# Kernel optimization log

Measured on AMD Instinct MI355X. Metric: run time of the kernel, lower is better.

Reference implementation:

```python
import jax, jax.numpy as jnp
import numpy as np

N_NODES = 50000
N_EDGES = 800000
DIM_IN, DIM_H, DIM_OUT = 128, 128, 64


def _init_linear(key, fan_in, fan_out):
    # kaiming-uniform-ish init, matches torch Linear scale
    lim = 1.0 / np.sqrt(fan_in)
    return jax.random.uniform(key, (fan_in, fan_out), jnp.float32, -lim, lim)


def setup_inputs() -> dict:
    key = jax.random.key(0)
    ks = jax.random.split(key, 12)
    x = jax.random.normal(ks[0], (N_NODES, DIM_IN), jnp.float32)
    edge_index = jax.random.randint(ks[1], (2, N_EDGES), 0, N_NODES, jnp.int32)
    dims = [(DIM_IN, DIM_H), (DIM_H, DIM_H), (DIM_H, DIM_OUT)]
    inp = {"x": x, "edge_index": edge_index}
    for i, (fi, fo) in enumerate(dims):
        inp[f"Wl{i}"] = _init_linear(ks[2 + 3 * i], fi, fo)   # neighbor transform
        inp[f"Wr{i}"] = _init_linear(ks[3 + 3 * i], fi, fo)   # root transform
        inp[f"b{i}"] = jnp.zeros((fo,), jnp.float32)
    return inp


def _sage_layer(x, src, dst, Wl, Wr, b):
    # mean aggregation of neighbor messages x[src] at destination nodes
    msg = x[src]                                              # [E, d]
    agg = jax.ops.segment_sum(msg, dst, num_segments=N_NODES)  # [N, d]
    cnt = jax.ops.segment_sum(jnp.ones((src.shape[0],), x.dtype), dst,
                              num_segments=N_NODES)
    mean = agg / jnp.maximum(cnt, 1.0)[:, None]               # isolated nodes -> 0
    return mean @ Wl + b + x @ Wr                              # SAGEConv


def reference(x, edge_index, Wl0, Wr0, b0, Wl1, Wr1, b1, Wl2, Wr2, b2):
    src, dst = edge_index[0], edge_index[1]
    layers = [(Wl0, Wr0, b0), (Wl1, Wr1, b1), (Wl2, Wr2, b2)]
    h = x
    for i, (Wl, Wr, b) in enumerate(layers):
        h = _sage_layer(h, src, dst, Wl, Wr, b)
        if i != len(layers) - 1:
            h = jax.nn.relu(h)  # dropout p=0.2 is identity in eval mode
    return jax.nn.log_softmax(h, axis=1), h
```

## Files before the change

kernel.cpp:

```cpp
#include <hip/hip_runtime.h>

#define N_NODES 50000
#define N_EDGES 800000
#define SCAN_BLOCKS 196
#define WIN 6250

typedef __attribute__((ext_vector_type(8))) short short8;
typedef __attribute__((ext_vector_type(4))) float f32x4;
typedef unsigned short ushort_t;
typedef unsigned int uint_t;

__device__ inline ushort_t f2bf(float f) {
    union { float f; uint_t u; } v; v.f = f;
    uint_t u = v.u;
    u += 0x7fffu + ((u >> 16) & 1u);
    return (ushort_t)(u >> 16);
}
__device__ inline float bflo(uint_t v) { return __uint_as_float(v << 16); }
__device__ inline float bfhi(uint_t v) { return __uint_as_float(v & 0xffff0000u); }
__device__ inline float bf2f(ushort_t v) { return __uint_as_float((uint_t)v << 16); }

__global__ void prep(const float* __restrict__ x, uint_t* __restrict__ x_bf_u,
                     const float* __restrict__ Wl0, const float* __restrict__ Wr0,
                     const float* __restrict__ Wl1, const float* __restrict__ Wr1,
                     const float* __restrict__ Wl2, const float* __restrict__ Wr2,
                     ushort_t* __restrict__ pk0, ushort_t* __restrict__ pk1,
                     ushort_t* __restrict__ pkz, int* __restrict__ cnt) {
    int b = blockIdx.x, tid = threadIdx.x;
    if (b < 6250) {
        int i = b * 256 + tid;
        float4 v = ((const float4*)x)[i];
        uint_t lo = (uint_t)f2bf(v.x) | ((uint_t)f2bf(v.y) << 16);
        uint_t hi = (uint_t)f2bf(v.z) | ((uint_t)f2bf(v.w) << 16);
        x_bf_u[i * 2] = lo; x_bf_u[i * 2 + 1] = hi;
    } else if (b < 6506) {
        int bb = b - 6250;
        const float* Wl = (bb < 128) ? Wl0 : Wl1;
        const float* Wr = (bb < 128) ? Wr0 : Wr1;
        ushort_t* out = (bb < 128) ? pk0 : pk1;
        int idx = (bb & 127) * 256 + tid;
        int j = idx & 7, l = (idx >> 3) & 63, t = (idx >> 9) & 7, ks = idx >> 12;
        int n = t * 16 + (l & 15);
        int k = ks * 32 + (l >> 4) * 8 + j;
        float w = (k < 128) ? Wl[k * 128 + n] : Wr[(k - 128) * 128 + n];
        out[idx] = f2bf(w);
    } else if (b < 6570) {
        int idx = (b - 6506) * 256 + tid;
        int j = idx & 7, l = (idx >> 3) & 63, t = (idx >> 9) & 7, ks = idx >> 12;
        int n = t * 16 + (l & 15);
        int k = ks * 32 + (l >> 4) * 8 + j;
        float w = (n < 64) ? Wl2[k * 64 + n] : Wr2[k * 64 + (n - 64)];
        pkz[idx] = f2bf(w);
    } else {
        int i = (b - 6570) * 256 + tid;
        if (i < 12500) ((int4*)cnt)[i] = make_int4(0, 0, 0, 0);
    }
}

__global__ void count_edges_mp(const int* __restrict__ ei, int* __restrict__ cnt) {
    int g = blockIdx.x & 7;
    int nb = gridDim.x >> 3;
    int bi = blockIdx.x >> 3;
    int lo = g * WIN;
    for (int e = bi * 256 + threadIdx.x; e < N_EDGES; e += nb * 256) {
        int d = ei[N_EDGES + e];
        if ((unsigned)(d - lo) < WIN) atomicAdd(&cnt[d], 1);
    }
}

__global__ void fill_csr_mp(const int* __restrict__ ei, int* __restrict__ cursor,
                            int* __restrict__ csr_src) {
    int g = blockIdx.x & 7;
    int nb = gridDim.x >> 3;
    int bi = blockIdx.x >> 3;
    int lo = g * WIN;
    for (int e = bi * 256 + threadIdx.x; e < N_EDGES; e += nb * 256) {
        int d = ei[N_EDGES + e];
        if ((unsigned)(d - lo) < WIN) {
            int p = atomicAdd(&cursor[d], 1);
            csr_src[p] = ei[e];
        }
    }
}

__global__ void scan_all(const int* __restrict__ cnt, int* __restrict__ rowstart,
                         int* __restrict__ cursor) {
    __shared__ int s[256];
    __shared__ int wsum[4];
    int t = threadIdx.x, b = blockIdx.x;
    int base = b * 256;
    int pre = 0;
    for (int i = t; i < base; i += 256) pre += cnt[i];
    for (int off = 32; off; off >>= 1) pre += __shfl_down(pre, off, 64);
    if ((t & 63) == 0) wsum[t >> 6] = pre;
    __syncthreads();
    int prefix_base = wsum[0] + wsum[1] + wsum[2] + wsum[3];
    int i = base + t;
    int v = (i < N_NODES) ? cnt[i] : 0;
    s[t] = v;
    __syncthreads();
    for (int off = 1; off < 256; off <<= 1) {
        int add = (t >= off) ? s[t - off] : 0;
        __syncthreads();
        s[t] += add;
        __syncthreads();
    }
    int excl = s[t] - v + prefix_base;
    if (i < N_NODES) { rowstart[i] = excl; cursor[i] = excl; }
    if (b == 0 && t == 0) rowstart[N_NODES] = N_EDGES;
}

__device__ inline void gather_mean(const uint_t* __restrict__ base,
                                   const int* __restrict__ rowstart,
                                   const int* __restrict__ csr_src,
                                   int node, int lane, float& ax, float& ay) {
    int s0 = rowstart[node], s1 = rowstart[node + 1];
    ax = 0.f; ay = 0.f;
    for (int b = s0; b < s1; b += 64) {
        int m = min(64, s1 - b);
        int idx = (lane < m) ? csr_src[b + lane] : 0;
        int j = 0;
        for (; j + 8 <= m; j += 8) {
            uint_t v0 = base[(size_t)__shfl(idx, j + 0, 64) * 64 + lane];
            uint_t v1 = base[(size_t)__shfl(idx, j + 1, 64) * 64 + lane];
            uint_t v2 = base[(size_t)__shfl(idx, j + 2, 64) * 64 + lane];
            uint_t v3 = base[(size_t)__shfl(idx, j + 3, 64) * 64 + lane];
            uint_t v4 = base[(size_t)__shfl(idx, j + 4, 64) * 64 + lane];
            uint_t v5 = base[(size_t)__shfl(idx, j + 5, 64) * 64 + lane];
            uint_t v6 = base[(size_t)__shfl(idx, j + 6, 64) * 64 + lane];
            uint_t v7 = base[(size_t)__shfl(idx, j + 7, 64) * 64 + lane];
            ax += ((bflo(v0) + bflo(v1)) + (bflo(v2) + bflo(v3)))
                + ((bflo(v4) + bflo(v5)) + (bflo(v6) + bflo(v7)));
            ay += ((bfhi(v0) + bfhi(v1)) + (bfhi(v2) + bfhi(v3)))
                + ((bfhi(v4) + bfhi(v5)) + (bfhi(v6) + bfhi(v7)));
        }
        for (; j < m; ++j) {
            uint_t v = base[(size_t)__shfl(idx, j, 64) * 64 + lane];
            ax += bflo(v);
            ay += bfhi(v);
        }
    }
    float inv = 1.0f / fmaxf((float)(s1 - s0), 1.0f);
    ax *= inv; ay *= inv;
}

template <bool CHAIN>
__global__ __launch_bounds__(256) void layer_fused(
    const uint_t* __restrict__ gsrc, const ushort_t* __restrict__ root,
    const int* __restrict__ rowstart, const int* __restrict__ csr_src,
    const ushort_t* __restrict__ Bpk, const float* __restrict__ bias1,
    const ushort_t* __restrict__ Bpkz, const float* __restrict__ bias2,
    ushort_t* __restrict__ h_out,
    ushort_t* __restrict__ z_bf, float* __restrict__ r_f32) {
    __shared__ ushort_t At[16 * 136];
    int lane = threadIdx.x & 63, wave = threadIdx.x >> 6;
    int nodeBase = blockIdx.x * 16;

    #pragma unroll
    for (int i = 0; i < 4; ++i) {
        int m = wave * 4 + i;
        int node = nodeBase + m;
        float ax = 0.f, ay = 0.f;
        if (node < N_NODES) gather_mean(gsrc, rowstart, csr_src, node, lane, ax, ay);
        ((uint_t*)(At + m * 136))[lane] = (uint_t)f2bf(ax) | ((uint_t)f2bf(ay) << 16);
    }
    __syncthreads();

    int row16 = lane & 15, quad = lane >> 4;
    const short8* bp = (const short8*)Bpk + lane;
    int rootRow = min(nodeBase + row16, N_NODES - 1);
    const ushort_t* rrow = root + (size_t)rootRow * 128;

    f32x4 acc[2];
    #pragma unroll
    for (int tt = 0; tt < 2; ++tt) { f32x4 z = {0.f, 0.f, 0.f, 0.f}; acc[tt] = z; }

    #pragma unroll
    for (int ks = 0; ks < 8; ++ks) {
        short8 afrag;
        if (ks < 4) afrag = *(const short8*)&At[row16 * 136 + ks * 32 + quad * 8];
        else        afrag = *(const short8*)(rrow + (ks - 4) * 32 + quad * 8);
        #pragma unroll
        for (int tt = 0; tt < 2; ++tt) {
            int t = wave * 2 + tt;
            short8 bfrag = bp[(ks * 8 + t) * 64];
            acc[tt] = __builtin_amdgcn_mfma_f32_16x16x32_bf16(afrag, bfrag, acc[tt], 0, 0, 0);
        }
    }

    if (!CHAIN) {
        #pragma unroll
        for (int tt = 0; tt < 2; ++tt) {
            int col = (wave * 2 + tt) * 16 + row16;
            float bv = bias1[col];
            #pragma unroll
            for (int r = 0; r < 4; ++r) {
                int row = nodeBase + quad * 4 + r;
                if (row < N_NODES) {
                    float v = fmaxf(acc[tt][r] + bv, 0.f);
                    h_out[(size_t)row * 128 + col] = f2bf(v);
                }
            }
        }
    } else {
        __syncthreads();
        #pragma unroll
        for (int tt = 0; tt < 2; ++tt) {
            int col = (wave * 2 + tt) * 16 + row16;
            float bv = bias1[col];
            #pragma unroll
            for (int r = 0; r < 4; ++r) {
                float v = fmaxf(acc[tt][r] + bv, 0.f);
                At[(quad * 4 + r) * 136 + col] = f2bf(v);
            }
        }
        __syncthreads();

        const short8* bpz = (const short8*)Bpkz + lane;
        f32x4 accz[2];
        #pragma unroll
        for (int tt = 0; tt < 2; ++tt) { f32x4 z = {0.f, 0.f, 0.f, 0.f}; accz[tt] = z; }

        #pragma unroll
        for (int ks = 0; ks < 4; ++ks) {
            short8 afrag = *(const short8*)&At[row16 * 136 + ks * 32 + quad * 8];
            #pragma unroll
            for (int tt = 0; tt < 2; ++tt) {
                int t = wave * 2 + tt;
                short8 bfrag = bpz[(ks * 8 + t) * 64];
                accz[tt] = __builtin_amdgcn_mfma_f32_16x16x32_bf16(afrag, bfrag, accz[tt], 0, 0, 0);
            }
        }

        #pragma unroll
        for (int tt = 0; tt < 2; ++tt) {
            int col = (wave * 2 + tt) * 16 + row16;
            #pragma unroll
            for (int r = 0; r < 4; ++r) {
                int row = nodeBase + quad * 4 + r;
                if (row < N_NODES) {
                    if (col < 64) z_bf[(size_t)row * 64 + col] = f2bf(accz[tt][r]);
                    else          r_f32[(size_t)row * 64 + (col - 64)] = accz[tt][r] + bias2[col - 64];
                }
            }
        }
    }
}

__global__ void final_agg_softmax(const ushort_t* __restrict__ z_bf,
                                  const float* __restrict__ r_f32,
                                  const int* __restrict__ rowstart,
                                  const int* __restrict__ csr_src,
                                  float* __restrict__ out) {
    int node = blockIdx.x * 4 + (threadIdx.x >> 6);
    int lane = threadIdx.x & 63;
    if (node >= N_NODES) return;
    int s0 = rowstart[node], s1 = rowstart[node + 1];
    float a = 0.f;
    for (int b = s0; b < s1; b += 64) {
        int m = min(64, s1 - b);
        int idx = (lane < m) ? csr_src[b + lane] : 0;
        int j = 0;
        for (; j + 8 <= m; j += 8) {
            float v0 = bf2f(z_bf[(size_t)__shfl(idx, j + 0, 64) * 64 + lane]);
            float v1 = bf2f(z_bf[(size_t)__shfl(idx, j + 1, 64) * 64 + lane]);
            float v2 = bf2f(z_bf[(size_t)__shfl(idx, j + 2, 64) * 64 + lane]);
            float v3 = bf2f(z_bf[(size_t)__shfl(idx, j + 3, 64) * 64 + lane]);
            float v4 = bf2f(z_bf[(size_t)__shfl(idx, j + 4, 64) * 64 + lane]);
            float v5 = bf2f(z_bf[(size_t)__shfl(idx, j + 5, 64) * 64 + lane]);
            float v6 = bf2f(z_bf[(size_t)__shfl(idx, j + 6, 64) * 64 + lane]);
            float v7 = bf2f(z_bf[(size_t)__shfl(idx, j + 7, 64) * 64 + lane]);
            a += ((v0 + v1) + (v2 + v3)) + ((v4 + v5) + (v6 + v7));
        }
        for (; j < m; ++j)
            a += bf2f(z_bf[(size_t)__shfl(idx, j, 64) * 64 + lane]);
    }
    float inv = 1.0f / fmaxf((float)(s1 - s0), 1.0f);
    float h = a * inv + r_f32[(size_t)node * 64 + lane];
    float mx = h;
    for (int off = 32; off; off >>= 1) mx = fmaxf(mx, __shfl_xor(mx, off, 64));
    float e = expf(h - mx);
    float s = e;
    for (int off = 32; off; off >>= 1) s += __shfl_xor(s, off, 64);
    float lse = mx + logf(s);
    out[(size_t)node * 64 + lane] = h - lse;
    out[(size_t)N_NODES * 64 + (size_t)node * 64 + lane] = h;
}

extern "C" void kernel_launch(void* const* d_in, const int* in_sizes, int n_in,
                              void* d_out, int out_size, void* d_ws, size_t ws_size,
                              hipStream_t stream) {
    const float* x  = (const float*)d_in[0];
    const int* ei   = (const int*)d_in[1];
    const float* Wl0 = (const float*)d_in[2];
    const float* Wr0 = (const float*)d_in[3];
    const float* b0  = (const float*)d_in[4];
    const float* Wl1 = (const float*)d_in[5];
    const float* Wr1 = (const float*)d_in[6];
    const float* b1  = (const float*)d_in[7];
    const float* Wl2 = (const float*)d_in[8];
    const float* Wr2 = (const float*)d_in[9];
    const float* b2  = (const float*)d_in[10];
    float* out = (float*)d_out;

    char* ws = (char*)d_ws;
    int* cnt      = (int*)(ws + 0x000000);
    int* rowstart = (int*)(ws + 0x040000);
    int* cursor   = (int*)(ws + 0x080000);
    int* csr_src  = (int*)(ws + 0x100000);
    ushort_t* pk0 = (ushort_t*)(ws + 0x420000);
    ushort_t* pk1 = (ushort_t*)(ws + 0x440000);
    ushort_t* pkz = (ushort_t*)(ws + 0x460000);
    ushort_t* x_bf = (ushort_t*)(ws + 0x0500000);
    ushort_t* h1   = (ushort_t*)(ws + 0x1F00000);
    ushort_t* z_bf = (ushort_t*)(ws + 0x1200000);
    float*    r_f32 = (float*)  (ws + 0x0500000);

    prep<<<6619, 256, 0, stream>>>(x, (uint_t*)x_bf, Wl0, Wr0, Wl1, Wr1, Wl2, Wr2,
                                   pk0, pk1, pkz, cnt);

    count_edges_mp<<<1024, 256, 0, stream>>>(ei, cnt);
    scan_all<<<SCAN_BLOCKS, 256, 0, stream>>>(cnt, rowstart, cursor);
    fill_csr_mp<<<1024, 256, 0, stream>>>(ei, cursor, csr_src);

    layer_fused<false><<<3125, 256, 0, stream>>>(
        (const uint_t*)x_bf, x_bf, rowstart, csr_src, pk0, b0,
        nullptr, nullptr, h1, nullptr, nullptr);

    layer_fused<true><<<3125, 256, 0, stream>>>(
        (const uint_t*)h1, h1, rowstart, csr_src, pk1, b1,
        pkz, b2, nullptr, z_bf, r_f32);

    final_agg_softmax<<<12500, 256, 0, stream>>>(z_bf, r_f32, rowstart, csr_src, out);
}
```

Measured before the change: 330.9 us.

## Gather neighbor rows with 16-byte vector loads and split waves across edges

Neighbor aggregation now loads each feature row as uint4 chunks, so one wave covers four edges at once (eight in the final kernel) and the partial sums are combined with cross-lane shuffles. The fused layer kernels move to 512 threads with 8 waves, each wave gathering 2 nodes and computing a single 16-column MFMA tile. The goal is fewer, wider memory transactions and more memory-level parallelism in the gather-bound phases. The cost is extra shuffle reductions, partly idle lanes on tails and for low-degree nodes, and higher register pressure under the new launch bounds.

New measurement: 337.4 us. Within noise of the previous version (+1.9%).

```diff
diff --git a/kernel.cpp b/kernel.cpp
--- a/kernel.cpp
+++ b/kernel.cpp
@@ -18,7 +18,9 @@
 }
 __device__ inline float bflo(uint_t v) { return __uint_as_float(v << 16); }
 __device__ inline float bfhi(uint_t v) { return __uint_as_float(v & 0xffff0000u); }
-__device__ inline float bf2f(ushort_t v) { return __uint_as_float((uint_t)v << 16); }
+__device__ inline uint_t packbf(float a, float b) {
+    return (uint_t)f2bf(a) | ((uint_t)f2bf(b) << 16);
+}
 
 __global__ void prep(const float* __restrict__ x, uint_t* __restrict__ x_bf_u,
                      const float* __restrict__ Wl0, const float* __restrict__ Wr0,
@@ -30,9 +32,8 @@
     if (b < 6250) {
         int i = b * 256 + tid;
         float4 v = ((const float4*)x)[i];
-        uint_t lo = (uint_t)f2bf(v.x) | ((uint_t)f2bf(v.y) << 16);
-        uint_t hi = (uint_t)f2bf(v.z) | ((uint_t)f2bf(v.w) << 16);
-        x_bf_u[i * 2] = lo; x_bf_u[i * 2 + 1] = hi;
+        x_bf_u[i * 2] = packbf(v.x, v.y);
+        x_bf_u[i * 2 + 1] = packbf(v.z, v.w);
     } else if (b < 6506) {
         int bb = b - 6250;
         const float* Wl = (bb < 128) ? Wl0 : Wl1;
@@ -110,59 +111,84 @@
     if (b == 0 && t == 0) rowstart[N_NODES] = N_EDGES;
 }
 
-__device__ inline void gather_mean(const uint_t* __restrict__ base,
-                                   const int* __restrict__ rowstart,
-                                   const int* __restrict__ csr_src,
-                                   int node, int lane, float& ax, float& ay) {
+__device__ inline void gather_mean4_128(const uint4* __restrict__ base,
+                                        const int* __restrict__ rowstart,
+                                        const int* __restrict__ csr,
+                                        int node, int lane, float* acc) {
     int s0 = rowstart[node], s1 = rowstart[node + 1];
-    ax = 0.f; ay = 0.f;
+    #pragma unroll
+    for (int k = 0; k < 8; ++k) acc[k] = 0.f;
+    int chunk = lane & 15, esel = lane >> 4;
     for (int b = s0; b < s1; b += 64) {
         int m = min(64, s1 - b);
-        int idx = (lane < m) ? csr_src[b + lane] : 0;
+        int idx = (lane < m) ? csr[b + lane] : 0;
         int j = 0;
-        for (; j + 8 <= m; j += 8) {
-            uint_t v0 = base[(size_t)__shfl(idx, j + 0, 64) * 64 + lane];
-            uint_t v1 = base[(size_t)__shfl(idx, j + 1, 64) * 64 + lane];
-            uint_t v2 = base[(size_t)__shfl(idx, j + 2, 64) * 64 + lane];
-            uint_t v3 = base[(size_t)__shfl(idx, j + 3, 64) * 64 + lane];
-            uint_t v4 = base[(size_t)__shfl(idx, j + 4, 64) * 64 + lane];
-            uint_t v5 = base[(size_t)__shfl(idx, j + 5, 64) * 64 + lane];
-            uint_t v6 = base[(size_t)__shfl(idx, j + 6, 64) * 64 + lane];
-            uint_t v7 = base[(size_t)__shfl(idx, j + 7, 64) * 64 + lane];
-            ax += ((bflo(v0) + bflo(v1)) + (bflo(v2) + bflo(v3)))
-                + ((bflo(v4) + bflo(v5)) + (bflo(v6) + bflo(v7)));
-            ay += ((bfhi(v0) + bfhi(v1)) + (bfhi(v2) + bfhi(v3)))
-                + ((bfhi(v4) + bfhi(v5)) + (bfhi(v6) + bfhi(v7)));
-        }
-        for (; j < m; ++j) {
-            uint_t v = base[(size_t)__shfl(idx, j, 64) * 64 + lane];
-            ax += bflo(v);
-            ay += bfhi(v);
+        for (; j + 16 <= m; j += 16) {
+            int i0 = __shfl(idx, j + esel, 64);
+            int i1 = __shfl(idx, j + 4 + esel, 64);
+            int i2 = __shfl(idx, j + 8 + esel, 64);
+            int i3 = __shfl(idx, j + 12 + esel, 64);
+            uint4 v0 = base[(size_t)i0 * 16 + chunk];
+            uint4 v1 = base[(size_t)i1 * 16 + chunk];
+            uint4 v2 = base[(size_t)i2 * 16 + chunk];
+            uint4 v3 = base[(size_t)i3 * 16 + chunk];
+            acc[0] += (bflo(v0.x) + bflo(v1.x)) + (bflo(v2.x) + bflo(v3.x));
+            acc[1] += (bfhi(v0.x) + bfhi(v1.x)) + (bfhi(v2.x) + bfhi(v3.x));
+            acc[2] += (bflo(v0.y) + bflo(v1.y)) + (bflo(v2.y) + bflo(v3.y));
+            acc[3] += (bfhi(v0.y) + bfhi(v1.y)) + (bfhi(v2.y) + bfhi(v3.y));
+            acc[4] += (bflo(v0.z) + bflo(v1.z)) + (bflo(v2.z) + bflo(v3.z));
+            acc[5] += (bfhi(v0.z) + bfhi(v1.z)) + (bfhi(v2.z) + bfhi(v3.z));
+            acc[6] += (bflo(v0.w) + bflo(v1.w)) + (bflo(v2.w) + bflo(v3.w));
+            acc[7] += (bfhi(v0.w) + bfhi(v1.w)) + (bfhi(v2.w) + bfhi(v3.w));
+        }
+        for (; j < m; j += 4) {
+            int e = j + esel;
+            int s = __shfl(idx, min(e, m - 1), 64);
+            if (e < m) {
+                uint4 v = base[(size_t)s * 16 + chunk];
+                acc[0] += bflo(v.x); acc[1] += bfhi(v.x);
+                acc[2] += bflo(v.y); acc[3] += bfhi(v.y);
+                acc[4] += bflo(v.z); acc[5] += bfhi(v.z);
+                acc[6] += bflo(v.w); acc[7] += bfhi(v.w);
+            }
         }
     }
     float inv = 1.0f / fmaxf((float)(s1 - s0), 1.0f);
-    ax *= inv; ay *= inv;
+    #pragma unroll
+    for (int k = 0; k < 8; ++k) {
+        acc[k] += __shfl_xor(acc[k], 16, 64);
+        acc[k] += __shfl_xor(acc[k], 32, 64);
+        acc[k] *= inv;
+    }
 }
 
 template <bool CHAIN>
-__global__ __launch_bounds__(256) void layer_fused(
-    const uint_t* __restrict__ gsrc, const ushort_t* __restrict__ root,
+__global__ __launch_bounds__(512, 8) void layer_fused(
+    const uint4* __restrict__ gsrc, const ushort_t* __restrict__ root,
     const int* __restrict__ rowstart, const int* __restrict__ csr_src,
     const ushort_t* __restrict__ Bpk, const float* __restrict__ bias1,
     const ushort_t* __restrict__ Bpkz, const float* __restrict__ bias2,
     ushort_t* __restrict__ h_out,
     ushort_t* __restrict__ z_bf, float* __restrict__ r_f32) {
-    __shared__ ushort_t At[16 * 136];
+    __shared__ __align__(16) ushort_t At[16 * 136];
     int lane = threadIdx.x & 63, wave = threadIdx.x >> 6;
     int nodeBase = blockIdx.x * 16;
-
-    #pragma unroll
-    for (int i = 0; i < 4; ++i) {
-        int m = wave * 4 + i;
+    int chunk = lane & 15;
+
+    #pragma unroll
+    for (int i = 0; i < 2; ++i) {
+        int m = wave * 2 + i;
         int node = nodeBase + m;
-        float ax = 0.f, ay = 0.f;
-        if (node < N_NODES) gather_mean(gsrc, rowstart, csr_src, node, lane, ax, ay);
-        ((uint_t*)(At + m * 136))[lane] = (uint_t)f2bf(ax) | ((uint_t)f2bf(ay) << 16);
+        float acc[8];
+        #pragma unroll
+        for (int k = 0; k < 8; ++k) acc[k] = 0.f;
+        if (node < N_NODES) gather_mean4_128(gsrc, rowstart, csr_src, node, lane, acc);
+        if (lane < 16) {
+            uint4 w;
+            w.x = packbf(acc[0], acc[1]); w.y = packbf(acc[2], acc[3]);
+            w.z = packbf(acc[4], acc[5]); w.w = packbf(acc[6], acc[7]);
+            *(uint4*)&At[m * 136 + chunk * 8] = w;
+        }
     }
     __syncthreads();
 
@@ -171,83 +197,58 @@
     int rootRow = min(nodeBase + row16, N_NODES - 1);
     const ushort_t* rrow = root + (size_t)rootRow * 128;
 
-    f32x4 acc[2];
-    #pragma unroll
-    for (int tt = 0; tt < 2; ++tt) { f32x4 z = {0.f, 0.f, 0.f, 0.f}; acc[tt] = z; }
-
+    f32x4 acc1 = {0.f, 0.f, 0.f, 0.f};
     #pragma unroll
     for (int ks = 0; ks < 8; ++ks) {
         short8 afrag;
         if (ks < 4) afrag = *(const short8*)&At[row16 * 136 + ks * 32 + quad * 8];
         else        afrag = *(const short8*)(rrow + (ks - 4) * 32 + quad * 8);
-        #pragma unroll
-        for (int tt = 0; tt < 2; ++tt) {
-            int t = wave * 2 + tt;
-            short8 bfrag = bp[(ks * 8 + t) * 64];
-            acc[tt] = __builtin_amdgcn_mfma_f32_16x16x32_bf16(afrag, bfrag, acc[tt], 0, 0, 0);
-        }
-    }
-
+        short8 bfrag = bp[(ks * 8 + wave) * 64];
+        acc1 = __builtin_amdgcn_mfma_f32_16x16x32_bf16(afrag, bfrag, acc1, 0, 0, 0);
+    }
+
+    int col = wave * 16 + row16;
     if (!CHAIN) {
-        #pragma unroll
-        for (int tt = 0; tt < 2; ++tt) {
-            int col = (wave * 2 + tt) * 16 + row16;
-            float bv = bias1[col];
-            #pragma unroll
-            for (int r = 0; r < 4; ++r) {
-                int row = nodeBase + quad * 4 + r;
-                if (row < N_NODES) {
-                    float v = fmaxf(acc[tt][r] + bv, 0.f);
-                    h_out[(size_t)row * 128 + col] = f2bf(v);
-                }
+        float bv = bias1[col];
+        #pragma unroll
+        for (int r = 0; r < 4; ++r) {
+            int row = nodeBase + quad * 4 + r;
+            if (row < N_NODES) {
+                float v = fmaxf(acc1[r] + bv, 0.f);
+                h_out[(size_t)row * 128 + col] = f2bf(v);
             }
         }
     } else {
         __syncthreads();
-        #pragma unroll
-        for (int tt = 0; tt < 2; ++tt) {
-            int col = (wave * 2 + tt) * 16 + row16;
-            float bv = bias1[col];
-            #pragma unroll
-            for (int r = 0; r < 4; ++r) {
-                float v = fmaxf(acc[tt][r] + bv, 0.f);
-                At[(quad * 4 + r) * 136 + col] = f2bf(v);
-            }
+        float bv = bias1[col];
+        #pragma unroll
+        for (int r = 0; r < 4; ++r) {
+            float v = fmaxf(acc1[r] + bv, 0.f);
+            At[(quad * 4 + r) * 136 + col] = f2bf(v);
         }
         __syncthreads();
 
         const short8* bpz = (const short8*)Bpkz + lane;
-        f32x4 accz[2];
-        #pragma unroll
-        for (int tt = 0; tt < 2; ++tt) { f32x4 z = {0.f, 0.f, 0.f, 0.f}; accz[tt] = z; }
-
+        f32x4 acc2 = {0.f, 0.f, 0.f, 0.f};
         #pragma unroll
         for (int ks = 0; ks < 4; ++ks) {
             short8 afrag = *(const short8*)&At[row16 * 136 + ks * 32 + quad * 8];
-            #pragma unroll
-            for (int tt = 0; tt < 2; ++tt) {
-                int t = wave * 2 + tt;
-                short8 bfrag = bpz[(ks * 8 + t) * 64];
-                accz[tt] = __builtin_amdgcn_mfma_f32_16x16x32_bf16(afrag, bfrag, accz[tt], 0, 0, 0);
+            short8 bfrag = bpz[(ks * 8 + wave) * 64];
+            acc2 = __builtin_amdgcn_mfma_f32_16x16x32_bf16(afrag, bfrag, acc2, 0, 0, 0);
+        }
+
+        #pragma unroll
+        for (int r = 0; r < 4; ++r) {
+            int row = nodeBase + quad * 4 + r;
+            if (row < N_NODES) {
+                if (col < 64) z_bf[(size_t)row * 64 + col] = f2bf(acc2[r]);
+                else          r_f32[(size_t)row * 64 + (col - 64)] = acc2[r] + bias2[col - 64];
             }
         }
-
-        #pragma unroll
-        for (int tt = 0; tt < 2; ++tt) {
-            int col = (wave * 2 + tt) * 16 + row16;
-            #pragma unroll
-            for (int r = 0; r < 4; ++r) {
-                int row = nodeBase + quad * 4 + r;
-                if (row < N_NODES) {
-                    if (col < 64) z_bf[(size_t)row * 64 + col] = f2bf(accz[tt][r]);
-                    else          r_f32[(size_t)row * 64 + (col - 64)] = accz[tt][r] + bias2[col - 64];
-                }
-            }
-        }
-    }
-}
-
-__global__ void final_agg_softmax(const ushort_t* __restrict__ z_bf,
+    }
+}
+
+__global__ void final_agg_softmax(const uint4* __restrict__ zb,
                                   const float* __restrict__ r_f32,
                                   const int* __restrict__ rowstart,
                                   const int* __restrict__ csr_src,
@@ -256,35 +257,81 @@
     int lane = threadIdx.x & 63;
     if (node >= N_NODES) return;
     int s0 = rowstart[node], s1 = rowstart[node + 1];
-    float a = 0.f;
+    int chunk = lane & 7, esel = lane >> 3;
+    float acc[8];
+    #pragma unroll
+    for (int k = 0; k < 8; ++k) acc[k] = 0.f;
     for (int b = s0; b < s1; b += 64) {
         int m = min(64, s1 - b);
         int idx = (lane < m) ? csr_src[b + lane] : 0;
         int j = 0;
-        for (; j + 8 <= m; j += 8) {
-            float v0 = bf2f(z_bf[(size_t)__shfl(idx, j + 0, 64) * 64 + lane]);
-            float v1 = bf2f(z_bf[(size_t)__shfl(idx, j + 1, 64) * 64 + lane]);
-            float v2 = bf2f(z_bf[(size_t)__shfl(idx, j + 2, 64) * 64 + lane]);
-            float v3 = bf2f(z_bf[(size_t)__shfl(idx, j + 3, 64) * 64 + lane]);
-            float v4 = bf2f(z_bf[(size_t)__shfl(idx, j + 4, 64) * 64 + lane]);
-            float v5 = bf2f(z_bf[(size_t)__shfl(idx, j + 5, 64) * 64 + lane]);
-            float v6 = bf2f(z_bf[(size_t)__shfl(idx, j + 6, 64) * 64 + lane]);
-            float v7 = bf2f(z_bf[(size_t)__shfl(idx, j + 7, 64) * 64 + lane]);
-            a += ((v0 + v1) + (v2 + v3)) + ((v4 + v5) + (v6 + v7));
-        }
-        for (; j < m; ++j)
-            a += bf2f(z_bf[(size_t)__shfl(idx, j, 64) * 64 + lane]);
+        for (; j + 32 <= m; j += 32) {
+            int i0 = __shfl(idx, j + esel, 64);
+            int i1 = __shfl(idx, j + 8 + esel, 64);
+            int i2 = __shfl(idx, j + 16 + esel, 64);
+            int i3 = __shfl(idx, j + 24 + esel, 64);
+            uint4 v0 = zb[(size_t)i0 * 8 + chunk];
+            uint4 v1 = zb[(size_t)i1 * 8 + chunk];
+            uint4 v2 = zb[(size_t)i2 * 8 + chunk];
+            uint4 v3 = zb[(size_t)i3 * 8 + chunk];
+            acc[0] += (bflo(v0.x) + bflo(v1.x)) + (bflo(v2.x) + bflo(v3.x));
+            acc[1] += (bfhi(v0.x) + bfhi(v1.x)) + (bfhi(v2.x) + bfhi(v3.x));
+            acc[2] += (bflo(v0.y) + bflo(v1.y)) + (bflo(v2.y) + bflo(v3.y));
+            acc[3] += (bfhi(v0.y) + bfhi(v1.y)) + (bfhi(v2.y) + bfhi(v3.y));
+            acc[4] += (bflo(v0.z) + bflo(v1.z)) + (bflo(v2.z) + bflo(v3.z));
+            acc[5] += (bfhi(v0.z) + bfhi(v1.z)) + (bfhi(v2.z) + bfhi(v3.z));
+            acc[6] += (bflo(v0.w) + bflo(v1.w)) + (bflo(v2.w) + bflo(v3.w));
+            acc[7] += (bfhi(v0.w) + bfhi(v1.w)) + (bfhi(v2.w) + bfhi(v3.w));
+        }
+        for (; j < m; j += 8) {
+            int e = j + esel;
+            int s = __shfl(idx, min(e, m - 1), 64);
+            if (e < m) {
+                uint4 v = zb[(size_t)s * 8 + chunk];
+                acc[0] += bflo(v.x); acc[1] += bfhi(v.x);
+                acc[2] += bflo(v.y); acc[3] += bfhi(v.y);
+                acc[4] += bflo(v.z); acc[5] += bfhi(v.z);
+                acc[6] += bflo(v.w); acc[7] += bfhi(v.w);
+            }
+        }
     }
     float inv = 1.0f / fmaxf((float)(s1 - s0), 1.0f);
-    float h = a * inv + r_f32[(size_t)node * 64 + lane];
-    float mx = h;
-    for (int off = 32; off; off >>= 1) mx = fmaxf(mx, __shfl_xor(mx, off, 64));
-    float e = expf(h - mx);
-    float s = e;
-    for (int off = 32; off; off >>= 1) s += __shfl_xor(s, off, 64);
+    #pragma unroll
+    for (int k = 0; k < 8; ++k) {
+        acc[k] += __shfl_xor(acc[k], 8, 64);
+        acc[k] += __shfl_xor(acc[k], 16, 64);
+        acc[k] += __shfl_xor(acc[k], 32, 64);
+    }
+    const float4* rp = (const float4*)(r_f32 + (size_t)node * 64 + chunk * 8);
+    float4 r0 = rp[0], r1 = rp[1];
+    float h[8];
+    h[0] = acc[0] * inv + r0.x; h[1] = acc[1] * inv + r0.y;
+    h[2] = acc[2] * inv + r0.z; h[3] = acc[3] * inv + r0.w;
+    h[4] = acc[4] * inv + r1.x; h[5] = acc[5] * inv + r1.y;
+    h[6] = acc[6] * inv + r1.z; h[7] = acc[7] * inv + r1.w;
+    float mx = h[0];
+    #pragma unroll
+    for (int k = 1; k < 8; ++k) mx = fmaxf(mx, h[k]);
+    mx = fmaxf(mx, __shfl_xor(mx, 1, 64));
+    mx = fmaxf(mx, __shfl_xor(mx, 2, 64));
+    mx = fmaxf(mx, __shfl_xor(mx, 4, 64));
+    float s = 0.f;
+    #pragma unroll
+    for (int k = 0; k < 8; ++k) s += expf(h[k] - mx);
+    s += __shfl_xor(s, 1, 64);
+    s += __shfl_xor(s, 2, 64);
+    s += __shfl_xor(s, 4, 64);
     float lse = mx + logf(s);
-    out[(size_t)node * 64 + lane] = h - lse;
-    out[(size_t)N_NODES * 64 + (size_t)node * 64 + lane] = h;
+    if (lane < 8) {
+        float4* o0 = (float4*)(out + (size_t)node * 64 + chunk * 8);
+        float4* o1 = (float4*)(out + (size_t)N_NODES * 64 + (size_t)node * 64 + chunk * 8);
+        float4 a = {h[0] - lse, h[1] - lse, h[2] - lse, h[3] - lse};
+        float4 bq = {h[4] - lse, h[5] - lse, h[6] - lse, h[7] - lse};
+        o0[0] = a; o0[1] = bq;
+        float4 c = {h[0], h[1], h[2], h[3]};
+        float4 d = {h[4], h[5], h[6], h[7]};
+        o1[0] = c; o1[1] = d;
+    }
 }
 
 extern "C" void kernel_launch(void* const* d_in, const int* in_sizes, int n_in,
@@ -323,13 +370,14 @@
     scan_all<<<SCAN_BLOCKS, 256, 0, stream>>>(cnt, rowstart, cursor);
     fill_csr_mp<<<1024, 256, 0, stream>>>(ei, cursor, csr_src);
 
-    layer_fused<false><<<3125, 256, 0, stream>>>(
-        (const uint_t*)x_bf, x_bf, rowstart, csr_src, pk0, b0,
+    layer_fused<false><<<3125, 512, 0, stream>>>(
+        (const uint4*)x_bf, x_bf, rowstart, csr_src, pk0, b0,
         nullptr, nullptr, h1, nullptr, nullptr);
 
-    layer_fused<true><<<3125, 256, 0, stream>>>(
-        (const uint_t*)h1, h1, rowstart, csr_src, pk1, b1,
+    layer_fused<true><<<3125, 512, 0, stream>>>(
+        (const uint4*)h1, h1, rowstart, csr_src, pk1, b1,
         pkz, b2, nullptr, z_bf, r_f32);
 
-    final_agg_softmax<<<12500, 256, 0, stream>>>(z_bf, r_f32, rowstart, csr_src, out);
-}
+    final_agg_softmax<<<12500, 256, 0, stream>>>((const uint4*)z_bf, r_f32,
+                                                 rowstart, csr_src, out);
+}
```
